# Kernel optimization log

Hardware: AMD Instinct MI355X
Metric: run time of the kernel (lower is better)

## Reference

```python
import math
import jax, jax.numpy as jnp
import numpy as np

NUM_TIERS = 3
TIER_SIZE = 50
GT_FACTOR = 2.0
MAX_REL = 8  # upper bound on relevant (gt) docs per query; labels built to respect this
B, D = 4096, 1000


def diff_fn(x):
    # 'maxmargin': relu(1 - x)
    return jax.nn.relu(1.0 - x)


def get_tier_inds(num_negatives):
    # tier_distance is None -> auto-spread tier centers
    mids = math.ceil((num_negatives - 2 * TIER_SIZE) / (NUM_TIERS - 1))
    return [0] + [TIER_SIZE // 2 + i * mids for i in range(1, NUM_TIERS - 1)] + [num_negatives - TIER_SIZE]


def setup_inputs() -> dict:
    key = jax.random.key(0)
    k1, k2 = jax.random.split(key)
    scores = jax.random.normal(k1, (B, D), dtype=jnp.float32)
    # n_i relevant docs per query in [1, MAX_REL]; labels[i,:n_i] = positions, rest -1
    n = jax.random.randint(k2, (B,), 1, MAX_REL + 1)
    cols = jnp.arange(D)
    labels = jnp.where(cols[None, :] < n[:, None], cols[None, :], -1).astype(jnp.int32)
    return {"scores": scores, "labels": labels}


def reference(scores, labels):
    Bq, Dq = scores.shape
    start_inds = get_tier_inds(Dq)
    loss = jnp.zeros(Bq, dtype=jnp.float32)
    # tiered pairwise diffs: each tier vs everything below it
    for t in range(NUM_TIERS - 1):
        s1 = scores[:, start_inds[t]:start_inds[t] + TIER_SIZE]      # (B, tier_size)
        s2 = scores[:, start_inds[t + 1]:]                            # (B, rest)
        d = diff_fn(s1[:, :, None] - s2[:, None, :])                  # (B, tier_size, rest)
        loss = loss + jnp.sum(d, axis=(1, 2)) / (s1.shape[1] * s2.shape[1])
    # ground-truth component (gt_function='same'), vectorized with masks instead of per-row loop
    n = jnp.sum(labels > -1, axis=1)                                  # (B,) num relevant per query
    rel_mask = jnp.arange(MAX_REL)[None, :] < n[:, None]              # (B, MAX_REL): j < n_i
    neg_mask = jnp.arange(Dq)[None, :] >= n[:, None]                  # (B, D): k >= n_i
    d = diff_fn(scores[:, :MAX_REL, None] - scores[:, None, :])       # (B, MAX_REL, D)
    mask = rel_mask[:, :, None] & neg_mask[:, None, :]
    gt_loss = jnp.sum(jnp.where(mask, d, 0.0), axis=(1, 2)) / Dq      # (B,)
    loss = loss + GT_FACTOR * gt_loss
    return jnp.mean(loss)  # reduction='mean'
```

## Files before the change

kernel.cpp:

```cpp
#include <hip/hip_runtime.h>
#include <float.h>


#define BQ 4096
#define DQ 1000
#define GRID 1024

__device__ __forceinline__ float bitonic_sort64(float v, int lane) {
    #pragma unroll
    for (int size = 2; size <= 64; size <<= 1) {
        #pragma unroll
        for (int stride = size >> 1; stride > 0; stride >>= 1) {
            float other = __shfl_xor(v, stride, 64);
            bool keep_min = (((lane & stride) == 0) == ((lane & size) == 0));
            v = keep_min ? fminf(v, other) : fmaxf(v, other);
        }
    }
    return v;
}

__device__ __forceinline__ float excl_scan50(float sv, int lane) {
    float x = (lane < 50) ? sv : 0.0f;
    float inc = x;
    #pragma unroll
    for (int off = 1; off < 64; off <<= 1) {
        float t = __shfl_up(inc, off, 64);
        if (lane >= off) inc += t;
    }
    return inc - x;
}

__device__ __forceinline__ float sorted_relu_sum(float x, float sv, float pre) {
    int c = 0;
    #pragma unroll
    for (int st = 32; st >= 1; st >>= 1) {
        float scv = __shfl(sv, c + st - 1, 64);
        c += (scv < x) ? st : 0;
    }
    float p = __shfl(pre, c, 64);
    return (float)c * x - p;
}

__global__ __launch_bounds__(256) void mtl_rows(const float* __restrict__ scores,
                                               const int* __restrict__ labels,
                                               float* __restrict__ partials) {
    const int tid  = threadIdx.x;
    const int lane = tid & 63;
    const int w    = tid >> 6;
    const int row  = blockIdx.x * 4 + w;
    const float* sr = scores + (size_t)row * DQ;

    __shared__ float wsum[4];

    float q[16];
    #pragma unroll
    for (int t = 0; t < 15; ++t) q[t] = sr[lane + 64 * t];
    q[15] = (lane < 40) ? sr[960 + lane] : 0.0f;

    int lv = -1;
    if (lane < 8) lv = labels[(size_t)row * DQ + lane];
    const int n = __popcll(__ballot(lv > -1));

    float sv0  = bitonic_sort64((lane < 50) ? q[0] : FLT_MAX, lane);
    float pre0 = excl_scan50(sv0, lane);

    float r1 = FLT_MAX;
    if (lane < 50) r1 = sr[475 + lane];
    float sv1  = bitonic_sort64(r1, lane);
    float pre1 = excl_scan50(sv1, lane);

    float tgt[16];
    #pragma unroll
    for (int t = 0; t < 16; ++t) tgt[t] = 0.0f;
    for (int k = 0; k < n; ++k) {
        float gk = 1.0f - __shfl(q[0], k, 64);
        #pragma unroll
        for (int t = 0; t < 16; ++t) tgt[t] += fmaxf(q[t] + gk, 0.0f);
    }
    float gts = (lane >= n) ? tgt[0] : 0.0f;
    #pragma unroll
    for (int t = 1; t < 15; ++t) gts += tgt[t];
    gts += (lane < 40) ? tgt[15] : 0.0f;
    float acc = gts * (2.0f / 1000.0f);

    float t0s = 0.0f;
    #pragma unroll
    for (int t = 7; t < 16; ++t) {
        float x = 1.0f + q[t];
        float val = sorted_relu_sum(x, sv0, pre0);
        bool act = (t == 7) ? (lane >= 27)
                 : (t == 15) ? (lane < 40)
                 : true;
        t0s += act ? val : 0.0f;
    }
    acc += t0s * (1.0f / 26250.0f);

    {
        float v14 = sorted_relu_sum(1.0f + q[14], sv1, pre1);
        acc += (lane >= 54) ? v14 * (1.0f / 2500.0f) : 0.0f;
        float v15 = sorted_relu_sum(1.0f + q[15], sv1, pre1);
        acc += (lane < 40) ? v15 * (1.0f / 2500.0f) : 0.0f;
    }

    #pragma unroll
    for (int off = 32; off > 0; off >>= 1) acc += __shfl_down(acc, off, 64);
    if (lane == 0) wsum[w] = acc;
    __syncthreads();
    if (tid == 0) partials[blockIdx.x] = wsum[0] + wsum[1] + wsum[2] + wsum[3];
}

__global__ __launch_bounds__(256) void mtl_reduce_kernel(const float* __restrict__ partials,
                                                         float* __restrict__ out) {
    __shared__ float wsum[4];
    const int tid  = threadIdx.x;
    float acc = partials[tid] + partials[tid + 256]
              + partials[tid + 512] + partials[tid + 768];
    #pragma unroll
    for (int off = 32; off > 0; off >>= 1) acc += __shfl_down(acc, off, 64);
    const int lane = tid & 63;
    const int wid  = tid >> 6;
    if (lane == 0) wsum[wid] = acc;
    __syncthreads();
    if (tid == 0) out[0] = (wsum[0] + wsum[1] + wsum[2] + wsum[3]) * (1.0f / (float)BQ);
}

extern "C" void kernel_launch(void* const* d_in, const int* in_sizes, int n_in,
                              void* d_out, int out_size, void* d_ws, size_t ws_size,
                              hipStream_t stream) {
    const float* scores = (const float*)d_in[0];
    const int*   labels = (const int*)d_in[1];
    float* partials = (float*)d_ws;
    float* out = (float*)d_out;

    mtl_rows<<<GRID, 256, 0, stream>>>(scores, labels, partials);
    mtl_reduce_kernel<<<1, 256, 0, stream>>>(partials, out);
}
```

Measured before the change: 79.63 us.

## Replace sort-and-search tier loss with brute-force readlane max accumulation

Drops the per-wave bitonic sort, prefix scan and binary-search shuffles. Tier and ground-truth pair sums are now computed directly with scalar readlane broadcasts and the identity relu(1+x-s)=max(x,s-1)-(s-1). Masked lanes are given -FLT_MAX so no per-term selects are needed. This trades many cross-lane shuffles for roughly 50x9 plus 50x2 max-add operations per lane, all on broadcast scalar operands.

```diff
diff --git a/kernel.cpp b/kernel.cpp
--- a/kernel.cpp
+++ b/kernel.cpp
@@ -6,39 +6,8 @@
 #define DQ 1000
 #define GRID 1024
 
-__device__ __forceinline__ float bitonic_sort64(float v, int lane) {
-    #pragma unroll
-    for (int size = 2; size <= 64; size <<= 1) {
-        #pragma unroll
-        for (int stride = size >> 1; stride > 0; stride >>= 1) {
-            float other = __shfl_xor(v, stride, 64);
-            bool keep_min = (((lane & stride) == 0) == ((lane & size) == 0));
-            v = keep_min ? fminf(v, other) : fmaxf(v, other);
-        }
-    }
-    return v;
-}
-
-__device__ __forceinline__ float excl_scan50(float sv, int lane) {
-    float x = (lane < 50) ? sv : 0.0f;
-    float inc = x;
-    #pragma unroll
-    for (int off = 1; off < 64; off <<= 1) {
-        float t = __shfl_up(inc, off, 64);
-        if (lane >= off) inc += t;
-    }
-    return inc - x;
-}
-
-__device__ __forceinline__ float sorted_relu_sum(float x, float sv, float pre) {
-    int c = 0;
-    #pragma unroll
-    for (int st = 32; st >= 1; st >>= 1) {
-        float scv = __shfl(sv, c + st - 1, 64);
-        c += (scv < x) ? st : 0;
-    }
-    float p = __shfl(pre, c, 64);
-    return (float)c * x - p;
+__device__ __forceinline__ float rdlane(float v, int l) {
+    return __int_as_float(__builtin_amdgcn_readlane(__float_as_int(v), l));
 }
 
 __global__ __launch_bounds__(256) void mtl_rows(const float* __restrict__ scores,
@@ -52,55 +21,77 @@
 
     __shared__ float wsum[4];
 
+    const float NEG = -FLT_MAX;
+
     float q[16];
     #pragma unroll
     for (int t = 0; t < 15; ++t) q[t] = sr[lane + 64 * t];
-    q[15] = (lane < 40) ? sr[960 + lane] : 0.0f;
+    q[15] = (lane < 40) ? sr[960 + lane] : NEG;
 
     int lv = -1;
     if (lane < 8) lv = labels[(size_t)row * DQ + lane];
     const int n = __popcll(__ballot(lv > -1));
 
-    float sv0  = bitonic_sort64((lane < 50) ? q[0] : FLT_MAX, lane);
-    float pre0 = excl_scan50(sv0, lane);
+    const float x7t0  = (lane >= 27) ? q[7]  : NEG;
+    const float x14t1 = (lane >= 54) ? q[14] : NEG;
+    const float x0g   = (lane >= n)  ? q[0]  : NEG;
 
-    float r1 = FLT_MAX;
-    if (lane < 50) r1 = sr[475 + lane];
-    float sv1  = bitonic_sort64(r1, lane);
-    float pre1 = excl_scan50(sv1, lane);
+    float a0[9];
+    #pragma unroll
+    for (int i = 0; i < 9; ++i) a0[i] = 0.0f;
+    float S0 = 0.0f;
+    #pragma unroll
+    for (int k = 0; k < 50; ++k) {
+        const float m = rdlane(q[0], k) - 1.0f;
+        S0 += m;
+        a0[0] += fmaxf(x7t0, m);
+        #pragma unroll
+        for (int t = 8; t < 15; ++t) a0[t - 7] += fmaxf(q[t], m);
+        a0[8] += fmaxf(q[15], m);
+    }
+    float t0 = ((a0[0] + a0[1]) + (a0[2] + a0[3]))
+             + ((a0[4] + a0[5]) + (a0[6] + a0[7])) + a0[8]
+             - 9.0f * S0;
 
-    float tgt[16];
+    float a1a = 0.0f, a1b = 0.0f, S1 = 0.0f;
     #pragma unroll
-    for (int t = 0; t < 16; ++t) tgt[t] = 0.0f;
+    for (int k = 0; k < 37; ++k) {
+        const float m = rdlane(q[7], 27 + k) - 1.0f;
+        S1 += m;
+        a1a += fmaxf(x14t1, m);
+        a1b += fmaxf(q[15], m);
+    }
+    #pragma unroll
+    for (int k = 0; k < 13; ++k) {
+        const float m = rdlane(q[8], k) - 1.0f;
+        S1 += m;
+        a1a += fmaxf(x14t1, m);
+        a1b += fmaxf(q[15], m);
+    }
+    float t1 = (a1a + a1b) - 2.0f * S1;
+
+    float gtacc = 0.0f, Sg = 0.0f;
     for (int k = 0; k < n; ++k) {
-        float gk = 1.0f - __shfl(q[0], k, 64);
+        const float m = rdlane(q[0], k) - 1.0f;
+        Sg += m;
+        float h0 = fmaxf(x0g,  m);
+        float h1 = fmaxf(q[1], m);
+        float h2 = fmaxf(q[2], m);
+        float h3 = fmaxf(q[3], m);
         #pragma unroll
-        for (int t = 0; t < 16; ++t) tgt[t] += fmaxf(q[t] + gk, 0.0f);
+        for (int t = 4; t < 16; t += 4) {
+            h0 += fmaxf(q[t],     m);
+            h1 += fmaxf(q[t + 1], m);
+            h2 += fmaxf(q[t + 2], m);
+            h3 += fmaxf(q[t + 3], m);
+        }
+        gtacc += (h0 + h1) + (h2 + h3);
     }
-    float gts = (lane >= n) ? tgt[0] : 0.0f;
-    #pragma unroll
-    for (int t = 1; t < 15; ++t) gts += tgt[t];
-    gts += (lane < 40) ? tgt[15] : 0.0f;
-    float acc = gts * (2.0f / 1000.0f);
+    float gt = gtacc - 16.0f * Sg;
 
-    float t0s = 0.0f;
-    #pragma unroll
-    for (int t = 7; t < 16; ++t) {
-        float x = 1.0f + q[t];
-        float val = sorted_relu_sum(x, sv0, pre0);
-        bool act = (t == 7) ? (lane >= 27)
-                 : (t == 15) ? (lane < 40)
-                 : true;
-        t0s += act ? val : 0.0f;
-    }
-    acc += t0s * (1.0f / 26250.0f);
-
-    {
-        float v14 = sorted_relu_sum(1.0f + q[14], sv1, pre1);
-        acc += (lane >= 54) ? v14 * (1.0f / 2500.0f) : 0.0f;
-        float v15 = sorted_relu_sum(1.0f + q[15], sv1, pre1);
-        acc += (lane < 40) ? v15 * (1.0f / 2500.0f) : 0.0f;
-    }
+    float acc = t0 * (1.0f / 26250.0f)
+              + t1 * (1.0f / 2500.0f)
+              + gt * (2.0f / 1000.0f);
 
     #pragma unroll
     for (int off = 32; off > 0; off >>= 1) acc += __shfl_down(acc, off, 64);
```

Result: slower. 84.72 us (+6.4%).
